# Optimization experiments

Hardware: AMD Instinct MI355X
Metric: run time of the kernel (lower is better)

## Reference

```python
import jax, jax.numpy as jnp
import numpy as np

N_NODES = 50000
N_EDGES = 800000
D = 96

def setup_inputs() -> dict:
    key = jax.random.key(0)
    ks = jax.random.split(key, 8)
    g = 0.1  # glorot-ish scale
    return {
        "x": jax.random.normal(ks[0], (N_NODES, D), jnp.float32),
        "edge_index": jax.random.randint(ks[1], (2, N_EDGES), 0, N_NODES, jnp.int64),
        "W1_root": jax.random.normal(ks[2], (D, D), jnp.float32) * g,
        "W1_nbr": jax.random.normal(ks[3], (D, D), jnp.float32) * g,
        "b1": jnp.zeros((D,), jnp.float32),
        "W2_root": jax.random.normal(ks[4], (D, D), jnp.float32) * g,
        "W2_nbr": jax.random.normal(ks[5], (D, D), jnp.float32) * g,
        "b2": jnp.zeros((D,), jnp.float32),
        "lin_w": jax.random.normal(ks[6], (D, 2 * D), jnp.float32) * g,
        "lin_b": jnp.zeros((D,), jnp.float32),
    }

def _conv(h, src, dst, W_root, W_nbr, b, neighbor_norm):
    # gather messages from source nodes, scatter-add into destination nodes
    agg = jax.ops.segment_sum(h[src], dst, num_segments=N_NODES)  # [N, D]
    if neighbor_norm:
        deg = jax.ops.segment_sum(jnp.ones_like(dst, dtype=h.dtype), dst,
                                  num_segments=N_NODES)
        agg = agg / jnp.maximum(deg, 1.0)[:, None]
    return h @ W_root + agg @ W_nbr + b

def reference(x, edge_index, W1_root, W1_nbr, b1, W2_root, W2_nbr, b2, lin_w, lin_b):
    src, dst = edge_index[0], edge_index[1]
    h1 = _conv(x, src, dst, W1_root, W1_nbr, b1, neighbor_norm=False)  # conv1, norm='None'
    h2 = _conv(h1, src, dst, W2_root, W2_nbr, b2, neighbor_norm=True)  # conv, neighbornorm
    # dropout is identity in eval mode; out=False so no global pooling
    cat = jnp.concatenate([h1, h2], axis=-1)  # [N, 2D]
    return jax.nn.relu(cat @ lin_w.T + lin_b)
```

## Files before the change

kernel.cpp:

```cpp
#include <hip/hip_runtime.h>

#define DN 96
#define NCHUNK 256

typedef __attribute__((ext_vector_type(8))) short bf16x8;
typedef __attribute__((ext_vector_type(4))) float f32x4;

__device__ __forceinline__ int edge_at(const void* ei, long long idx, int use64) {
    if (use64) return (int)((const long long*)ei)[idx];
    return ((const int*)ei)[idx];
}

__device__ __forceinline__ unsigned short f2bf(float f) {
    unsigned int u = __float_as_uint(f);
    return (unsigned short)((u + 0x7fffu + ((u >> 16) & 1u)) >> 16);
}

__global__ __launch_bounds__(256) void preprocess(
        const float* __restrict__ x, unsigned int* __restrict__ xb,
        const void* __restrict__ ei, unsigned int* __restrict__ eidx,
        int* __restrict__ hist,
        const float* __restrict__ W1r, const float* __restrict__ W1n,
        const float* __restrict__ W2r, const float* __restrict__ W2n,
        const float* __restrict__ lw, unsigned short* __restrict__ WT,
        long long E, long long CE, int nbuck, int NP) {
    __shared__ int lh[800];
    __shared__ int flag;
    int c = blockIdx.x, tid = threadIdx.x;

    if (tid == 0) flag = 1;
    for (int b = tid; b < nbuck; b += 256) lh[b] = 0;
    __syncthreads();
    if (((const unsigned int*)ei)[2 * tid + 1] != 0u) atomicAnd(&flag, 0);
    __syncthreads();
    int use64 = flag;

    long long beg = (long long)c * CE;
    long long end = beg + CE; if (end > E) end = E;
    for (long long e = beg + tid; e < end; e += 256) {
        int s = edge_at(ei, e, use64);
        int d = edge_at(ei, E + e, use64);
        eidx[e] = (unsigned int)s | ((unsigned int)d << 16);
        atomicAdd(&lh[d >> 6], 1);
    }
    __syncthreads();
    for (int b = tid; b < nbuck; b += 256)
        hist[(size_t)c * nbuck + b] = lh[b];

    int gstride = gridDim.x * 256;
    for (int i = c * 256 + tid; i < NP; i += gstride) {
        float2 v = *(const float2*)(x + 2 * (size_t)i);
        xb[i] = (unsigned int)f2bf(v.x) | ((unsigned int)f2bf(v.y) << 16);
    }

    for (int j = c * 256 + tid; j < 3 * DN * 192; j += gstride) {
        int w = j / (DN * 192);
        int r = j % (DN * 192);
        int jj = r / 192, k = r % 192;
        float v;
        if (w == 0)      v = (k < DN) ? W1r[(size_t)k * DN + jj] : W1n[(size_t)(k - DN) * DN + jj];
        else if (w == 1) v = (k < DN) ? W2r[(size_t)k * DN + jj] : W2n[(size_t)(k - DN) * DN + jj];
        else             v = lw[r];
        WT[j] = f2bf(v);
    }
}

__global__ void bucket_scan(const int* __restrict__ hist, int* __restrict__ pos_rel,
                            int* __restrict__ btot, int nbuck) {
    __shared__ int wsum[4];
    int b = blockIdx.x, tid = threadIdx.x;
    int lane = tid & 63, wid = tid >> 6;
    int v = hist[(size_t)tid * nbuck + b];
    int sv = v;
#pragma unroll
    for (int off = 1; off < 64; off <<= 1) {
        int t = __shfl_up(sv, off, 64);
        if (lane >= off) sv += t;
    }
    if (lane == 63) wsum[wid] = sv;
    __syncthreads();
    int woff = 0;
    for (int w = 0; w < wid; ++w) woff += wsum[w];
    pos_rel[(size_t)tid * nbuck + b] = woff + sv - v;
    if (tid == 255) btot[b] = woff + sv;
}

__global__ void scan_excl(int* data, int n) {
    __shared__ int swsum[16];
    int tid = threadIdx.x;
    int lane = tid & 63, wid = tid >> 6;
    int carry = 0;
    for (int base = 0; base < n; base += 1024) {
        int i = base + tid;
        int v = (i < n) ? data[i] : 0;
        int sv = v;
#pragma unroll
        for (int off = 1; off < 64; off <<= 1) {
            int t = __shfl_up(sv, off, 64);
            if (lane >= off) sv += t;
        }
        __syncthreads();
        if (lane == 63) swsum[wid] = sv;
        __syncthreads();
        if (tid < 16) {
            int wv = swsum[tid];
#pragma unroll
            for (int off = 1; off < 16; off <<= 1) {
                int t = __shfl_up(wv, off, 16);
                if (tid >= off) wv += t;
            }
            swsum[tid] = wv;
        }
        __syncthreads();
        int woff = (wid > 0) ? swsum[wid - 1] : 0;
        int excl = carry + woff + sv - v;
        if (i < n) data[i] = excl;
        carry += swsum[15];
        __syncthreads();
    }
    if (tid == 0) data[n] = carry;
}

__global__ void scatter_grouped(const unsigned int* __restrict__ eidx, long long E,
                                const int* __restrict__ pos_rel,
                                const int* __restrict__ bstart,
                                unsigned int* __restrict__ packed,
                                int nbuck, long long CE) {
    __shared__ int cur[800];
    int c = blockIdx.x, tid = threadIdx.x;
    for (int b = tid; b < nbuck; b += 256)
        cur[b] = pos_rel[(size_t)c * nbuck + b] + bstart[b];
    __syncthreads();
    long long beg = (long long)c * CE;
    long long end = beg + CE; if (end > E) end = E;
    for (long long e = beg + tid; e < end; e += 256) {
        unsigned int u = eidx[e];
        int src = (int)(u & 0xFFFFu);
        int dst = (int)(u >> 16);
        int b = dst >> 6;
        int p = atomicAdd(&cur[b], 1);
        packed[p] = (unsigned int)src | ((unsigned int)(dst & 63) << 16);
    }
}

__global__ void bucket_sort(const unsigned int* __restrict__ packed,
                            const int* __restrict__ bstart,
                            unsigned short* __restrict__ csr_src,
                            int* __restrict__ rowptr, int n, int nbuck) {
    __shared__ int bin[64];
    __shared__ int cur[64];
    int b = blockIdx.x, tid = threadIdx.x;
    int beg = bstart[b], end = bstart[b + 1];
    if (tid < 64) bin[tid] = 0;
    __syncthreads();
    for (int i = beg + tid; i < end; i += 256)
        atomicAdd(&bin[packed[i] >> 16], 1);
    __syncthreads();
    if (tid < 64) {
        int v = bin[tid];
        int sv = v;
#pragma unroll
        for (int off = 1; off < 64; off <<= 1) {
            int t = __shfl_up(sv, off, 64);
            if (tid >= off) sv += t;
        }
        int excl = sv - v;
        cur[tid] = beg + excl;
        int node = b * 64 + tid;
        if (node < n) rowptr[node] = beg + excl;
    }
    __syncthreads();
    for (int i = beg + tid; i < end; i += 256) {
        unsigned int p = packed[i];
        int q = atomicAdd(&cur[p >> 16], 1);
        csr_src[q] = (unsigned short)(p & 0xFFFFu);
    }
    if (b == nbuck - 1 && tid == 0) rowptr[n] = end;
}

__device__ __forceinline__ void acc_row(float* acc, uint4 v) {
    unsigned int u;
    u = v.x; acc[0] += __uint_as_float(u << 16); acc[1] += __uint_as_float(u & 0xffff0000u);
    u = v.y; acc[2] += __uint_as_float(u << 16); acc[3] += __uint_as_float(u & 0xffff0000u);
    u = v.z; acc[4] += __uint_as_float(u << 16); acc[5] += __uint_as_float(u & 0xffff0000u);
    u = v.w; acc[6] += __uint_as_float(u << 16); acc[7] += __uint_as_float(u & 0xffff0000u);
}

__global__ void aggregate(const unsigned int* __restrict__ in, unsigned int* __restrict__ out,
                          const int* __restrict__ rowptr,
                          const unsigned short* __restrict__ srcs,
                          int n, int normalize) {
    int t = blockIdx.x * blockDim.x + threadIdx.x;
    if (t >= n * 12) return;
    int node = t / 12, c = t % 12;
    int beg = rowptr[node], end = rowptr[node + 1];
    float acc[8];
#pragma unroll
    for (int j = 0; j < 8; ++j) acc[j] = 0.f;
    int i = beg;
    for (; i + 8 <= end; i += 8) {
        int s[8];
        uint4 v[8];
#pragma unroll
        for (int j = 0; j < 8; ++j) s[j] = srcs[i + j];
#pragma unroll
        for (int j = 0; j < 8; ++j) v[j] = *(const uint4*)(in + (size_t)s[j] * 48 + c * 4);
#pragma unroll
        for (int j = 0; j < 8; ++j) acc_row(acc, v[j]);
    }
    if (i + 4 <= end) {
        int s0 = srcs[i], s1 = srcs[i + 1], s2 = srcs[i + 2], s3 = srcs[i + 3];
        uint4 v0 = *(const uint4*)(in + (size_t)s0 * 48 + c * 4);
        uint4 v1 = *(const uint4*)(in + (size_t)s1 * 48 + c * 4);
        uint4 v2 = *(const uint4*)(in + (size_t)s2 * 48 + c * 4);
        uint4 v3 = *(const uint4*)(in + (size_t)s3 * 48 + c * 4);
        acc_row(acc, v0); acc_row(acc, v1); acc_row(acc, v2); acc_row(acc, v3);
        i += 4;
    }
    for (; i < end; ++i) {
        uint4 v = *(const uint4*)(in + (size_t)srcs[i] * 48 + c * 4);
        acc_row(acc, v);
    }
    if (normalize) {
        float inv = 1.0f / fmaxf((float)(end - beg), 1.0f);
#pragma unroll
        for (int j = 0; j < 8; ++j) acc[j] *= inv;
    }
    uint4 r;
    r.x = (unsigned int)f2bf(acc[0]) | ((unsigned int)f2bf(acc[1]) << 16);
    r.y = (unsigned int)f2bf(acc[2]) | ((unsigned int)f2bf(acc[3]) << 16);
    r.z = (unsigned int)f2bf(acc[4]) | ((unsigned int)f2bf(acc[5]) << 16);
    r.w = (unsigned int)f2bf(acc[6]) | ((unsigned int)f2bf(acc[7]) << 16);
    *(uint4*)(out + (size_t)node * 48 + c * 4) = r;
}

__global__ __launch_bounds__(256) void gemm_mfma(
        const unsigned short* __restrict__ Abf, const unsigned short* __restrict__ Bbf,
        const unsigned short* __restrict__ WT, const float* __restrict__ bias,
        float* __restrict__ outf, unsigned short* __restrict__ outb,
        int n, int dorelu) {
    __shared__ unsigned int WTl[DN * 100];
    int tid = threadIdx.x;
    const unsigned int* WTg = (const unsigned int*)WT;
    for (int i = tid; i < DN * 96; i += 256) {
        int j = i / 96, m = i - j * 96;
        WTl[j * 100 + m] = WTg[i];
    }
    __syncthreads();

    int wid = tid >> 6, lane = tid & 63;
    int lg = lane >> 4, lr = lane & 15;
    int rowbase = blockIdx.x * 128 + wid * 32;

    f32x4 acc[2][6];
#pragma unroll
    for (int rt = 0; rt < 2; ++rt)
#pragma unroll
        for (int ct = 0; ct < 6; ++ct) acc[rt][ct] = (f32x4){0.f, 0.f, 0.f, 0.f};

    const unsigned short* WTs = (const unsigned short*)WTl;
#pragma unroll
    for (int kt = 0; kt < 6; ++kt) {
        const unsigned short* src = (kt < 3) ? Abf : Bbf;
        int kk = (kt < 3 ? kt : kt - 3) * 32 + lg * 8;
        bf16x8 afrag[2];
#pragma unroll
        for (int rt = 0; rt < 2; ++rt) {
            int row = rowbase + rt * 16 + lr;
            if (row >= n) row = n - 1;
            afrag[rt] = *(const bf16x8*)(src + (size_t)row * DN + kk);
        }
        int koff = kt * 32 + lg * 8;
#pragma unroll
        for (int ct = 0; ct < 6; ++ct) {
            bf16x8 bfrag = *(const bf16x8*)(WTs + (ct * 16 + lr) * 200 + koff);
            acc[0][ct] = __builtin_amdgcn_mfma_f32_16x16x32_bf16(afrag[0], bfrag, acc[0][ct], 0, 0, 0);
            acc[1][ct] = __builtin_amdgcn_mfma_f32_16x16x32_bf16(afrag[1], bfrag, acc[1][ct], 0, 0, 0);
        }
    }

#pragma unroll
    for (int ct = 0; ct < 6; ++ct) {
        int col = ct * 16 + lr;
        float bv = bias[col];
#pragma unroll
        for (int rt = 0; rt < 2; ++rt)
#pragma unroll
            for (int r = 0; r < 4; ++r) {
                int row = rowbase + rt * 16 + lg * 4 + r;
                if (row < n) {
                    float v = acc[rt][ct][r] + bv;
                    if (dorelu) v = fmaxf(v, 0.f);
                    if (outf) outf[(size_t)row * DN + col] = v;
                    if (outb) outb[(size_t)row * DN + col] = f2bf(v);
                }
            }
    }
}

__global__ __launch_bounds__(256) void gemm_fused(
        const unsigned short* __restrict__ h1, const unsigned short* __restrict__ agg,
        const unsigned short* __restrict__ WT2, const float* __restrict__ b2,
        const unsigned short* __restrict__ WT3, const float* __restrict__ lb,
        float* __restrict__ out, int n) {
    __shared__ unsigned int WTl[DN * 100];
    __shared__ unsigned short h2t[4][32][98];
    int tid = threadIdx.x, wid = tid >> 6, lane = tid & 63;
    int lg = lane >> 4, lr = lane & 15;
    int rowbase = blockIdx.x * 128 + wid * 32;

    const unsigned int* WTg2 = (const unsigned int*)WT2;
    for (int i = tid; i < DN * 96; i += 256) {
        int j = i / 96, m = i - j * 96;
        WTl[j * 100 + m] = WTg2[i];
    }
    __syncthreads();

    f32x4 acc[2][6];
#pragma unroll
    for (int rt = 0; rt < 2; ++rt)
#pragma unroll
        for (int ct = 0; ct < 6; ++ct) acc[rt][ct] = (f32x4){0.f, 0.f, 0.f, 0.f};

    const unsigned short* WTs = (const unsigned short*)WTl;
    bf16x8 afragA[2][3];
#pragma unroll
    for (int kt = 0; kt < 6; ++kt) {
        bf16x8 afrag[2];
#pragma unroll
        for (int rt = 0; rt < 2; ++rt) {
            int row = rowbase + rt * 16 + lr;
            if (row >= n) row = n - 1;
            if (kt < 3) {
                afrag[rt] = *(const bf16x8*)(h1 + (size_t)row * DN + kt * 32 + lg * 8);
                afragA[rt][kt] = afrag[rt];
            } else {
                afrag[rt] = *(const bf16x8*)(agg + (size_t)row * DN + (kt - 3) * 32 + lg * 8);
            }
        }
        int koff = kt * 32 + lg * 8;
#pragma unroll
        for (int ct = 0; ct < 6; ++ct) {
            bf16x8 bfrag = *(const bf16x8*)(WTs + (ct * 16 + lr) * 200 + koff);
            acc[0][ct] = __builtin_amdgcn_mfma_f32_16x16x32_bf16(afrag[0], bfrag, acc[0][ct], 0, 0, 0);
            acc[1][ct] = __builtin_amdgcn_mfma_f32_16x16x32_bf16(afrag[1], bfrag, acc[1][ct], 0, 0, 0);
        }
    }

#pragma unroll
    for (int ct = 0; ct < 6; ++ct) {
        float bv = b2[ct * 16 + lr];
#pragma unroll
        for (int rt = 0; rt < 2; ++rt)
#pragma unroll
            for (int r = 0; r < 4; ++r)
                h2t[wid][rt * 16 + lg * 4 + r][ct * 16 + lr] = f2bf(acc[rt][ct][r] + bv);
    }
    __syncthreads();

    const unsigned int* WTg3 = (const unsigned int*)WT3;
    for (int i = tid; i < DN * 96; i += 256) {
        int j = i / 96, m = i - j * 96;
        WTl[j * 100 + m] = WTg3[i];
    }
    __syncthreads();

    f32x4 acc2[2][6];
#pragma unroll
    for (int rt = 0; rt < 2; ++rt)
#pragma unroll
        for (int ct = 0; ct < 6; ++ct) acc2[rt][ct] = (f32x4){0.f, 0.f, 0.f, 0.f};

#pragma unroll
    for (int kt = 0; kt < 6; ++kt) {
        bf16x8 afrag[2];
#pragma unroll
        for (int rt = 0; rt < 2; ++rt) {
            if (kt < 3) afrag[rt] = afragA[rt][kt];
            else        afrag[rt] = *(const bf16x8*)(&h2t[wid][rt * 16 + lr][(kt - 3) * 32 + lg * 8]);
        }
        int koff = kt * 32 + lg * 8;
#pragma unroll
        for (int ct = 0; ct < 6; ++ct) {
            bf16x8 bfrag = *(const bf16x8*)(WTs + (ct * 16 + lr) * 200 + koff);
            acc2[0][ct] = __builtin_amdgcn_mfma_f32_16x16x32_bf16(afrag[0], bfrag, acc2[0][ct], 0, 0, 0);
            acc2[1][ct] = __builtin_amdgcn_mfma_f32_16x16x32_bf16(afrag[1], bfrag, acc2[1][ct], 0, 0, 0);
        }
    }

#pragma unroll
    for (int ct = 0; ct < 6; ++ct) {
        int col = ct * 16 + lr;
        float bv = lb[col];
#pragma unroll
        for (int rt = 0; rt < 2; ++rt)
#pragma unroll
            for (int r = 0; r < 4; ++r) {
                int row = rowbase + rt * 16 + lg * 4 + r;
                if (row < n)
                    out[(size_t)row * DN + col] = fmaxf(acc2[rt][ct][r] + bv, 0.f);
            }
    }
}

extern "C" void kernel_launch(void* const* d_in, const int* in_sizes, int n_in,
                              void* d_out, int out_size, void* d_ws, size_t ws_size,
                              hipStream_t stream) {
    const float* x   = (const float*)d_in[0];
    const void*  ei  = d_in[1];
    const float* W1r = (const float*)d_in[2];
    const float* W1n = (const float*)d_in[3];
    const float* b1  = (const float*)d_in[4];
    const float* W2r = (const float*)d_in[5];
    const float* W2n = (const float*)d_in[6];
    const float* b2  = (const float*)d_in[7];
    const float* lw  = (const float*)d_in[8];
    const float* lb  = (const float*)d_in[9];
    float* out = (float*)d_out;

    const int N = in_sizes[0] / DN;
    const long long E = in_sizes[1] / 2;
    const int NBUCK = (N + 63) / 64;
    const long long CE = (E + NCHUNK - 1) / NCHUNK;
    const size_t NP = (size_t)N * 48;

    unsigned int* xb   = (unsigned int*)d_ws;
    unsigned int* h1b  = xb + NP;
    unsigned int* aggb = h1b + NP;
    unsigned short* WT = (unsigned short*)(aggb + NP);
    unsigned short* WT1 = WT;
    unsigned short* WT2 = WT + DN * 192;
    unsigned short* WT3 = WT2 + DN * 192;
    unsigned int* eidx = (unsigned int*)(WT3 + DN * 192);
    int* hist   = (int*)(eidx + E);
    int* pos    = hist + NCHUNK * NBUCK;
    int* btot   = pos + NCHUNK * NBUCK;
    int* rowptr = btot + NBUCK + 1;
    unsigned int* packed = (unsigned int*)(rowptr + N + 1);
    unsigned short* csr_src = (unsigned short*)(packed + E);

    preprocess<<<NCHUNK, 256, 0, stream>>>(x, xb, ei, eidx, hist,
                                           W1r, W1n, W2r, W2n, lw, WT,
                                           E, CE, NBUCK, (int)NP);
    bucket_scan<<<NBUCK, 256, 0, stream>>>(hist, pos, btot, NBUCK);
    scan_excl<<<1, 1024, 0, stream>>>(btot, NBUCK);
    scatter_grouped<<<NCHUNK, 256, 0, stream>>>(eidx, E, pos, btot, packed, NBUCK, CE);
    bucket_sort<<<NBUCK, 256, 0, stream>>>(packed, btot, csr_src, rowptr, N, NBUCK);

    int ab = (N * 12 + 255) / 256;
    int gb = (N + 127) / 128;

    aggregate<<<ab, 256, 0, stream>>>(xb, aggb, rowptr, csr_src, N, 0);
    gemm_mfma<<<gb, 256, 0, stream>>>((const unsigned short*)xb, (const unsigned short*)aggb,
                                      WT1, b1, (float*)0, (unsigned short*)h1b, N, 0);
    aggregate<<<ab, 256, 0, stream>>>(h1b, aggb, rowptr, csr_src, N, 1);
    gemm_fused<<<gb, 256, 0, stream>>>((const unsigned short*)h1b, (const unsigned short*)aggb,
                                       WT2, b2, WT3, lb, out, N);
}
```

Measured before the change: 122.6 us.

## Fuse neighbor aggregation into GEMM kernels via shared-memory staging

Removes the two standalone aggregate kernels and computes each block's 128-row neighbor sums directly inside the GEMM kernels, staging them in LDS instead of writing and rereading a global agg buffer. This eliminates two launches and a full N×96 bf16 round trip per layer. In exchange each GEMM block now spends serial gather time before its MFMA work, only 256 threads per 128 rows do the gather, and occupancy may drop from the extra LDS. The h2 staging buffer is reused from the agg tile with an added barrier.

```diff
diff --git a/kernel.cpp b/kernel.cpp
--- a/kernel.cpp
+++ b/kernel.cpp
@@ -186,14 +186,9 @@
     u = v.w; acc[6] += __uint_as_float(u << 16); acc[7] += __uint_as_float(u & 0xffff0000u);
 }
 
-__global__ void aggregate(const unsigned int* __restrict__ in, unsigned int* __restrict__ out,
-                          const int* __restrict__ rowptr,
-                          const unsigned short* __restrict__ srcs,
-                          int n, int normalize) {
-    int t = blockIdx.x * blockDim.x + threadIdx.x;
-    if (t >= n * 12) return;
-    int node = t / 12, c = t % 12;
-    int beg = rowptr[node], end = rowptr[node + 1];
+__device__ __forceinline__ uint4 agg_gather(const unsigned int* __restrict__ in,
+                                            const unsigned short* __restrict__ srcs,
+                                            int beg, int end, int c, int normalize) {
     float acc[8];
 #pragma unroll
     for (int j = 0; j < 8; ++j) acc[j] = 0.f;
@@ -231,26 +226,40 @@
     r.y = (unsigned int)f2bf(acc[2]) | ((unsigned int)f2bf(acc[3]) << 16);
     r.z = (unsigned int)f2bf(acc[4]) | ((unsigned int)f2bf(acc[5]) << 16);
     r.w = (unsigned int)f2bf(acc[6]) | ((unsigned int)f2bf(acc[7]) << 16);
-    *(uint4*)(out + (size_t)node * 48 + c * 4) = r;
-}
-
-__global__ __launch_bounds__(256) void gemm_mfma(
-        const unsigned short* __restrict__ Abf, const unsigned short* __restrict__ Bbf,
+    return r;
+}
+
+__global__ __launch_bounds__(256) void gemm_conv(
+        const unsigned short* __restrict__ Abf,
         const unsigned short* __restrict__ WT, const float* __restrict__ bias,
-        float* __restrict__ outf, unsigned short* __restrict__ outb,
-        int n, int dorelu) {
+        const int* __restrict__ rowptr, const unsigned short* __restrict__ srcs,
+        unsigned short* __restrict__ outb, int n, int normalize) {
     __shared__ unsigned int WTl[DN * 100];
+    __shared__ unsigned int aggt[128 * 50];
     int tid = threadIdx.x;
+    int block_row0 = blockIdx.x * 128;
+
     const unsigned int* WTg = (const unsigned int*)WT;
     for (int i = tid; i < DN * 96; i += 256) {
         int j = i / 96, m = i - j * 96;
         WTl[j * 100 + m] = WTg[i];
     }
+
+    const unsigned int* inw = (const unsigned int*)Abf;
+    for (int w = tid; w < 128 * 12; w += 256) {
+        int ln = w / 12, c = w - ln * 12;
+        int node = block_row0 + ln;
+        uint4 r = make_uint4(0u, 0u, 0u, 0u);
+        if (node < n)
+            r = agg_gather(inw, srcs, rowptr[node], rowptr[node + 1], c, normalize);
+        unsigned int* d = &aggt[ln * 50 + c * 4];
+        d[0] = r.x; d[1] = r.y; d[2] = r.z; d[3] = r.w;
+    }
     __syncthreads();
 
     int wid = tid >> 6, lane = tid & 63;
     int lg = lane >> 4, lr = lane & 15;
-    int rowbase = blockIdx.x * 128 + wid * 32;
+    int rowbase = block_row0 + wid * 32;
 
     f32x4 acc[2][6];
 #pragma unroll
@@ -261,14 +270,17 @@
     const unsigned short* WTs = (const unsigned short*)WTl;
 #pragma unroll
     for (int kt = 0; kt < 6; ++kt) {
-        const unsigned short* src = (kt < 3) ? Abf : Bbf;
-        int kk = (kt < 3 ? kt : kt - 3) * 32 + lg * 8;
         bf16x8 afrag[2];
 #pragma unroll
         for (int rt = 0; rt < 2; ++rt) {
-            int row = rowbase + rt * 16 + lr;
-            if (row >= n) row = n - 1;
-            afrag[rt] = *(const bf16x8*)(src + (size_t)row * DN + kk);
+            if (kt < 3) {
+                int row = rowbase + rt * 16 + lr;
+                if (row >= n) row = n - 1;
+                afrag[rt] = *(const bf16x8*)(Abf + (size_t)row * DN + kt * 32 + lg * 8);
+            } else {
+                int lrow = wid * 32 + rt * 16 + lr;
+                afrag[rt] = *(const bf16x8*)((const unsigned short*)&aggt[lrow * 50 + (kt - 3) * 16 + lg * 4]);
+            }
         }
         int koff = kt * 32 + lg * 8;
 #pragma unroll
@@ -288,32 +300,41 @@
 #pragma unroll
             for (int r = 0; r < 4; ++r) {
                 int row = rowbase + rt * 16 + lg * 4 + r;
-                if (row < n) {
-                    float v = acc[rt][ct][r] + bv;
-                    if (dorelu) v = fmaxf(v, 0.f);
-                    if (outf) outf[(size_t)row * DN + col] = v;
-                    if (outb) outb[(size_t)row * DN + col] = f2bf(v);
-                }
+                if (row < n)
+                    outb[(size_t)row * DN + col] = f2bf(acc[rt][ct][r] + bv);
             }
     }
 }
 
 __global__ __launch_bounds__(256) void gemm_fused(
-        const unsigned short* __restrict__ h1, const unsigned short* __restrict__ agg,
+        const unsigned short* __restrict__ h1,
         const unsigned short* __restrict__ WT2, const float* __restrict__ b2,
         const unsigned short* __restrict__ WT3, const float* __restrict__ lb,
+        const int* __restrict__ rowptr, const unsigned short* __restrict__ srcs,
         float* __restrict__ out, int n) {
     __shared__ unsigned int WTl[DN * 100];
-    __shared__ unsigned short h2t[4][32][98];
+    __shared__ unsigned int aggt[128 * 50];
     int tid = threadIdx.x, wid = tid >> 6, lane = tid & 63;
     int lg = lane >> 4, lr = lane & 15;
-    int rowbase = blockIdx.x * 128 + wid * 32;
+    int block_row0 = blockIdx.x * 128;
+    int rowbase = block_row0 + wid * 32;
 
     const unsigned int* WTg2 = (const unsigned int*)WT2;
     for (int i = tid; i < DN * 96; i += 256) {
         int j = i / 96, m = i - j * 96;
         WTl[j * 100 + m] = WTg2[i];
     }
+
+    const unsigned int* inw = (const unsigned int*)h1;
+    for (int w = tid; w < 128 * 12; w += 256) {
+        int ln = w / 12, c = w - ln * 12;
+        int node = block_row0 + ln;
+        uint4 r = make_uint4(0u, 0u, 0u, 0u);
+        if (node < n)
+            r = agg_gather(inw, srcs, rowptr[node], rowptr[node + 1], c, 1);
+        unsigned int* d = &aggt[ln * 50 + c * 4];
+        d[0] = r.x; d[1] = r.y; d[2] = r.z; d[3] = r.w;
+    }
     __syncthreads();
 
     f32x4 acc[2][6];
@@ -329,13 +350,14 @@
         bf16x8 afrag[2];
 #pragma unroll
         for (int rt = 0; rt < 2; ++rt) {
-            int row = rowbase + rt * 16 + lr;
-            if (row >= n) row = n - 1;
             if (kt < 3) {
+                int row = rowbase + rt * 16 + lr;
+                if (row >= n) row = n - 1;
                 afrag[rt] = *(const bf16x8*)(h1 + (size_t)row * DN + kt * 32 + lg * 8);
                 afragA[rt][kt] = afrag[rt];
             } else {
-                afrag[rt] = *(const bf16x8*)(agg + (size_t)row * DN + (kt - 3) * 32 + lg * 8);
+                int lrow = wid * 32 + rt * 16 + lr;
+                afrag[rt] = *(const bf16x8*)((const unsigned short*)&aggt[lrow * 50 + (kt - 3) * 16 + lg * 4]);
             }
         }
         int koff = kt * 32 + lg * 8;
@@ -346,7 +368,9 @@
             acc[1][ct] = __builtin_amdgcn_mfma_f32_16x16x32_bf16(afrag[1], bfrag, acc[1][ct], 0, 0, 0);
         }
     }
-
+    __syncthreads();
+
+    unsigned short* h2t = (unsigned short*)aggt;
 #pragma unroll
     for (int ct = 0; ct < 6; ++ct) {
         float bv = b2[ct * 16 + lr];
@@ -354,10 +378,9 @@
         for (int rt = 0; rt < 2; ++rt)
 #pragma unroll
             for (int r = 0; r < 4; ++r)
-                h2t[wid][rt * 16 + lg * 4 + r][ct * 16 + lr] = f2bf(acc[rt][ct][r] + bv);
-    }
-    __syncthreads();
-
+                h2t[(wid * 32 + rt * 16 + lg * 4 + r) * 98 + ct * 16 + lr] =
+                    f2bf(acc[rt][ct][r] + bv);
+    }
     const unsigned int* WTg3 = (const unsigned int*)WT3;
     for (int i = tid; i < DN * 96; i += 256) {
         int j = i / 96, m = i - j * 96;
@@ -377,7 +400,7 @@
 #pragma unroll
         for (int rt = 0; rt < 2; ++rt) {
             if (kt < 3) afrag[rt] = afragA[rt][kt];
-            else        afrag[rt] = *(const bf16x8*)(&h2t[wid][rt * 16 + lr][(kt - 3) * 32 + lg * 8]);
+            else        afrag[rt] = *(const bf16x8*)(&h2t[(wid * 32 + rt * 16 + lr) * 98 + (kt - 3) * 32 + lg * 8]);
         }
         int koff = kt * 32 + lg * 8;
 #pragma unroll
@@ -426,8 +449,7 @@
 
     unsigned int* xb   = (unsigned int*)d_ws;
     unsigned int* h1b  = xb + NP;
-    unsigned int* aggb = h1b + NP;
-    unsigned short* WT = (unsigned short*)(aggb + NP);
+    unsigned short* WT = (unsigned short*)(h1b + NP);
     unsigned short* WT1 = WT;
     unsigned short* WT2 = WT + DN * 192;
     unsigned short* WT3 = WT2 + DN * 192;
@@ -447,13 +469,10 @@
     scatter_grouped<<<NCHUNK, 256, 0, stream>>>(eidx, E, pos, btot, packed, NBUCK, CE);
     bucket_sort<<<NBUCK, 256, 0, stream>>>(packed, btot, csr_src, rowptr, N, NBUCK);
 
-    int ab = (N * 12 + 255) / 256;
     int gb = (N + 127) / 128;
 
-    aggregate<<<ab, 256, 0, stream>>>(xb, aggb, rowptr, csr_src, N, 0);
-    gemm_mfma<<<gb, 256, 0, stream>>>((const unsigned short*)xb, (const unsigned short*)aggb,
-                                      WT1, b1, (float*)0, (unsigned short*)h1b, N, 0);
-    aggregate<<<ab, 256, 0, stream>>>(h1b, aggb, rowptr, csr_src, N, 1);
-    gemm_fused<<<gb, 256, 0, stream>>>((const unsigned short*)h1b, (const unsigned short*)aggb,
-                                       WT2, b2, WT3, lb, out, N);
-}
+    gemm_conv<<<gb, 256, 0, stream>>>((const unsigned short*)xb, WT1, b1,
+                                      rowptr, csr_src, (unsigned short*)h1b, N, 0);
+    gemm_fused<<<gb, 256, 0, stream>>>((const unsigned short*)h1b, WT2, b2, WT3, lb,
+                                       rowptr, csr_src, out, N);
+}
```

Result: slower. 137.7 us (+12.3%).
